# Optimization experiments

Hardware: AMD Instinct MI355X
Metric: run time of the kernel (lower is better)

Reference implementation:

```python
import jax, jax.numpy as jnp
import numpy as np

KERNEL_SIZE = 65
STRIDE = 1
PAD = (KERNEL_SIZE - 1) // 2  # padding='same'


def setup_inputs() -> dict:
    key = jax.random.key(0)
    k1, k2 = jax.random.split(key)
    B, Cin, T = 8, 512, 512
    out_size = (Cin + 2 * PAD - (KERNEL_SIZE - 1) - 1) // STRIDE + 1  # 512
    x = jax.random.normal(k1, (B, Cin, T), dtype=jnp.float32)
    # per-output-position weights, init randn/sqrt(K) as in the torch module
    weights = jax.random.normal(k2, (out_size, 1, KERNEL_SIZE), dtype=jnp.float32) / jnp.sqrt(
        jnp.float32(KERNEL_SIZE)
    )
    bias = jnp.zeros((out_size, 1), dtype=jnp.float32)
    return {"x": x, "weights": weights, "bias": bias}


def reference(x, weights, bias):
    # x: (B, Cin, T) -> output (B, T, out_size)
    out_size, _, K = weights.shape
    xt = jnp.swapaxes(x, 1, 2)                       # (B, T, Cin)
    xp = jnp.pad(xt, ((0, 0), (0, 0), (PAD, PAD)))   # (B, T, Cin + 2p)
    # sliding windows over the (padded) channel axis: (out_size, K) gather indices
    idx = jnp.arange(out_size)[:, None] * STRIDE + jnp.arange(K)[None, :]
    win = xp[:, :, idx]                              # (B, T, out_size, K)
    # locally-connected matvec: distinct K-vector per output position o
    y = jnp.einsum("btok,ok->bto", win, weights[:, 0, :])
    y = y + bias[:, 0]                               # (B, T, out_size)
    return y
```

## Files before the change

kernel.cpp:

```cpp
#include <hip/hip_runtime.h>

#define B_    8
#define C_    512
#define T_    512
#define O_    512
#define K_    65
#define PAD_  32

#define O_TILE 32
#define T_TILE 128
#define J_     8
#define NW     4
#define ROWS   (O_TILE + 2 * PAD_)
#define NR     (J_ + 2 * PAD_)
#define YPITCH 36

#define NOG       (O_ / J_)
#define WT_ELEMS  (NOG * NR * J_)

__global__ __launch_bounds__(256) void wt_prep(const float* __restrict__ w,
                                               float* __restrict__ wt) {
    int e = blockIdx.x * 256 + threadIdx.x;
    if (e >= WT_ELEMS) return;
    int og  = e / (NR * J_);
    int rem = e % (NR * J_);
    int r   = rem / J_;
    int j   = rem % J_;
    int k   = r - j;
    float v = 0.0f;
    if (k >= 0 && k < K_) v = w[(og * J_ + j) * K_ + k];
    wt[e] = v;
}

template <bool USE_WT>
__global__ __launch_bounds__(256) void conv_main(const float* __restrict__ x,
                                                 const float* __restrict__ w,
                                                 const float* __restrict__ bias,
                                                 const float* __restrict__ wt,
                                                 float* __restrict__ out) {
    __shared__ float smem[ROWS * T_TILE];

    const int tid = threadIdx.x;
    const int bid = blockIdx.x;
    const int b   = bid >> 6;
    const int rem = bid & 63;
    const int ob  = rem >> 2;
    const int tb  = rem & 3;
    const int t0  = tb * T_TILE;
    const int c_base = ob * O_TILE - PAD_;

    {
        const float* xb = x + (size_t)b * (C_ * T_);
        const int l32 = tid & 31;
        const int rg  = tid >> 5;
        #pragma unroll
        for (int rr = 0; rr < ROWS / 8; ++rr) {
            const int row = rr * 8 + rg;
            const int c   = c_base + row;
            float4 v = make_float4(0.f, 0.f, 0.f, 0.f);
            if (c >= 0 && c < C_)
                v = *(const float4*)(xb + c * T_ + t0 + l32 * 4);
            *(float4*)(&smem[row * T_TILE + l32 * 4]) = v;
        }
    }
    __syncthreads();

    const int lane  = tid & 63;
    const int wu    = __builtin_amdgcn_readfirstlane(tid >> 6);
    const int og    = ob * NW + wu;
    const int obase = og * J_;

    float2 acc[J_];
    #pragma unroll
    for (int j = 0; j < J_; ++j) {
        const float bj = bias[obase + j];
        acc[j] = make_float2(bj, bj);
    }

    const int tl = lane * 2;
    const float* wt_base = wt + (size_t)og * (NR * J_);

    for (int r = 0; r < NR; ++r) {
        const float2 xv = *(const float2*)(&smem[(wu * J_ + r) * T_TILE + tl]);
        float w8[J_];
        if (USE_WT) {
            const float4 wa = *(const float4*)(wt_base + r * J_);
            const float4 wb = *(const float4*)(wt_base + r * J_ + 4);
            w8[0] = wa.x; w8[1] = wa.y; w8[2] = wa.z; w8[3] = wa.w;
            w8[4] = wb.x; w8[5] = wb.y; w8[6] = wb.z; w8[7] = wb.w;
        } else {
            #pragma unroll
            for (int j = 0; j < J_; ++j) {
                const int k = r - j;
                w8[j] = (k >= 0 && k < K_) ? w[(obase + j) * K_ + k] : 0.f;
            }
        }
        #pragma unroll
        for (int j = 0; j < J_; ++j) {
            acc[j].x += w8[j] * xv.x;
            acc[j].y += w8[j] * xv.y;
        }
    }

    __syncthreads();

    {
        const int olb = wu * J_;
        #pragma unroll
        for (int j = 0; j < J_; ++j) {
            smem[tl * YPITCH + olb + j]       = acc[j].x;
            smem[(tl + 1) * YPITCH + olb + j] = acc[j].y;
        }
    }
    __syncthreads();

    {
        float* ob_out = out + (size_t)b * (T_ * O_) + (size_t)t0 * O_ + ob * O_TILE;
        const int ol   = (tid & 7) * 4;
        const int trow = tid >> 3;
        #pragma unroll
        for (int p = 0; p < 4; ++p) {
            const int t_local = p * 32 + trow;
            const float4 v = *(const float4*)(&smem[t_local * YPITCH + ol]);
            *(float4*)(ob_out + (size_t)t_local * O_ + ol) = v;
        }
    }
}

extern "C" void kernel_launch(void* const* d_in, const int* in_sizes, int n_in,
                              void* d_out, int out_size, void* d_ws, size_t ws_size,
                              hipStream_t stream) {
    const float* x    = (const float*)d_in[0];
    const float* w    = (const float*)d_in[1];
    const float* bias = (const float*)d_in[2];
    float* out = (float*)d_out;
    float* wt  = (float*)d_ws;

    const int nblocks = B_ * (O_ / O_TILE) * (T_ / T_TILE);

    if (ws_size >= (size_t)WT_ELEMS * sizeof(float)) {
        wt_prep<<<(WT_ELEMS + 255) / 256, 256, 0, stream>>>(w, wt);
        conv_main<true><<<nblocks, 256, 0, stream>>>(x, w, bias, wt, out);
    } else {
        conv_main<false><<<nblocks, 256, 0, stream>>>(x, w, bias, w, out);
    }
}
```

Before: 74.96 us.

## Fuse banded weight prep into conv kernel via per-block LDS weight tile

Removes the separate wt_prep launch and global workspace; each block now builds its own zero-padded banded weight tile in shared memory alongside the x tile. The inner loop reads weights from LDS instead of global memory and is unrolled by 4, and accumulator stores to the transpose buffer become float4 writes. This saves one kernel launch and a global round trip for the weights. In exchange, every block redundantly gathers weights with integer div/mod, and the LDS footprint grows, which may affect occupancy.

```diff
diff --git a/kernel.cpp b/kernel.cpp
--- a/kernel.cpp
+++ b/kernel.cpp
@@ -15,30 +15,17 @@
 #define NR     (J_ + 2 * PAD_)
 #define YPITCH 36
 
-#define NOG       (O_ / J_)
-#define WT_ELEMS  (NOG * NR * J_)
+#define XTILE_ELEMS (ROWS * T_TILE)
+#define WT_TILE     (NW * NR * J_)
 
-__global__ __launch_bounds__(256) void wt_prep(const float* __restrict__ w,
-                                               float* __restrict__ wt) {
-    int e = blockIdx.x * 256 + threadIdx.x;
-    if (e >= WT_ELEMS) return;
-    int og  = e / (NR * J_);
-    int rem = e % (NR * J_);
-    int r   = rem / J_;
-    int j   = rem % J_;
-    int k   = r - j;
-    float v = 0.0f;
-    if (k >= 0 && k < K_) v = w[(og * J_ + j) * K_ + k];
-    wt[e] = v;
-}
-
-template <bool USE_WT>
-__global__ __launch_bounds__(256) void conv_main(const float* __restrict__ x,
-                                                 const float* __restrict__ w,
-                                                 const float* __restrict__ bias,
-                                                 const float* __restrict__ wt,
-                                                 float* __restrict__ out) {
-    __shared__ float smem[ROWS * T_TILE];
+__global__ __launch_bounds__(256, 2)
+void conv_fused(const float* __restrict__ x,
+                const float* __restrict__ w,
+                const float* __restrict__ bias,
+                float* __restrict__ out) {
+    __shared__ float smem[XTILE_ELEMS + WT_TILE];
+    float* xs  = smem;
+    float* wts = smem + XTILE_ELEMS;
 
     const int tid = threadIdx.x;
     const int bid = blockIdx.x;
@@ -60,15 +47,30 @@
             float4 v = make_float4(0.f, 0.f, 0.f, 0.f);
             if (c >= 0 && c < C_)
                 v = *(const float4*)(xb + c * T_ + t0 + l32 * 4);
-            *(float4*)(&smem[row * T_TILE + l32 * 4]) = v;
+            *(float4*)(&xs[row * T_TILE + l32 * 4]) = v;
+        }
+    }
+
+    {
+        #pragma unroll
+        for (int p = 0; p < WT_TILE / 256; ++p) {
+            const int e  = p * 256 + tid;
+            const int wg = e / (NR * J_);
+            const int r2 = e % (NR * J_);
+            const int r  = r2 >> 3;
+            const int j  = r2 & 7;
+            const int o  = (ob * NW + wg) * J_ + j;
+            const int k  = r - j;
+            float v = 0.f;
+            if (k >= 0 && k < K_) v = w[o * K_ + k];
+            wts[e] = v;
         }
     }
     __syncthreads();
 
     const int lane  = tid & 63;
     const int wu    = __builtin_amdgcn_readfirstlane(tid >> 6);
-    const int og    = ob * NW + wu;
-    const int obase = og * J_;
+    const int obase = (ob * NW + wu) * J_;
 
     float2 acc[J_];
     #pragma unroll
@@ -78,39 +80,32 @@
     }
 
     const int tl = lane * 2;
-    const float* wt_base = wt + (size_t)og * (NR * J_);
+    const float* xrow = xs + (wu * J_) * T_TILE + tl;
+    const float* wrow = wts + wu * (NR * J_);
 
+    #pragma unroll 4
     for (int r = 0; r < NR; ++r) {
-        const float2 xv = *(const float2*)(&smem[(wu * J_ + r) * T_TILE + tl]);
-        float w8[J_];
-        if (USE_WT) {
-            const float4 wa = *(const float4*)(wt_base + r * J_);
-            const float4 wb = *(const float4*)(wt_base + r * J_ + 4);
-            w8[0] = wa.x; w8[1] = wa.y; w8[2] = wa.z; w8[3] = wa.w;
-            w8[4] = wb.x; w8[5] = wb.y; w8[6] = wb.z; w8[7] = wb.w;
-        } else {
-            #pragma unroll
-            for (int j = 0; j < J_; ++j) {
-                const int k = r - j;
-                w8[j] = (k >= 0 && k < K_) ? w[(obase + j) * K_ + k] : 0.f;
-            }
-        }
-        #pragma unroll
-        for (int j = 0; j < J_; ++j) {
-            acc[j].x += w8[j] * xv.x;
-            acc[j].y += w8[j] * xv.y;
-        }
+        const float2 xv = *(const float2*)(xrow + r * T_TILE);
+        const float4 wa = *(const float4*)(wrow + r * J_);
+        const float4 wb = *(const float4*)(wrow + r * J_ + 4);
+        acc[0].x += wa.x * xv.x;  acc[0].y += wa.x * xv.y;
+        acc[1].x += wa.y * xv.x;  acc[1].y += wa.y * xv.y;
+        acc[2].x += wa.z * xv.x;  acc[2].y += wa.z * xv.y;
+        acc[3].x += wa.w * xv.x;  acc[3].y += wa.w * xv.y;
+        acc[4].x += wb.x * xv.x;  acc[4].y += wb.x * xv.y;
+        acc[5].x += wb.y * xv.x;  acc[5].y += wb.y * xv.y;
+        acc[6].x += wb.z * xv.x;  acc[6].y += wb.z * xv.y;
+        acc[7].x += wb.w * xv.x;  acc[7].y += wb.w * xv.y;
     }
 
     __syncthreads();
 
     {
         const int olb = wu * J_;
-        #pragma unroll
-        for (int j = 0; j < J_; ++j) {
-            smem[tl * YPITCH + olb + j]       = acc[j].x;
-            smem[(tl + 1) * YPITCH + olb + j] = acc[j].y;
-        }
+        *(float4*)(&smem[tl * YPITCH + olb])           = make_float4(acc[0].x, acc[1].x, acc[2].x, acc[3].x);
+        *(float4*)(&smem[tl * YPITCH + olb + 4])       = make_float4(acc[4].x, acc[5].x, acc[6].x, acc[7].x);
+        *(float4*)(&smem[(tl + 1) * YPITCH + olb])     = make_float4(acc[0].y, acc[1].y, acc[2].y, acc[3].y);
+        *(float4*)(&smem[(tl + 1) * YPITCH + olb + 4]) = make_float4(acc[4].y, acc[5].y, acc[6].y, acc[7].y);
     }
     __syncthreads();
 
@@ -134,14 +129,7 @@
     const float* w    = (const float*)d_in[1];
     const float* bias = (const float*)d_in[2];
     float* out = (float*)d_out;
-    float* wt  = (float*)d_ws;
 
     const int nblocks = B_ * (O_ / O_TILE) * (T_ / T_TILE);
-
-    if (ws_size >= (size_t)WT_ELEMS * sizeof(float)) {
-        wt_prep<<<(WT_ELEMS + 255) / 256, 256, 0, stream>>>(w, wt);
-        conv_main<true><<<nblocks, 256, 0, stream>>>(x, w, bias, wt, out);
-    } else {
-        conv_main<false><<<nblocks, 256, 0, stream>>>(x, w, bias, w, out);
-    }
+    conv_fused<<<nblocks, 256, 0, stream>>>(x, w, bias, out);
 }
```

Result: no change. 75.54 us (+0.8%).
